# Performance work log

Measured on AMD Instinct MI355X. Metric: run time of the kernel, lower is better.

Reference implementation:

```python
import jax, jax.numpy as jnp
import numpy as np

B, L, E, H = 4, 2048, 512, 8
HD = E // H
EPS = 1e-6


def setup_inputs() -> dict:
    key = jax.random.key(0)
    ks = jax.random.split(key, 9)
    s = 0.02
    return {
        "query": jax.random.normal(ks[0], (B, L, E), dtype=jnp.float32),
        "Wq": jax.random.normal(ks[1], (E, E), dtype=jnp.float32) * s,
        "bq": jnp.zeros((E,), dtype=jnp.float32),
        "Wk": jax.random.normal(ks[2], (E, E), dtype=jnp.float32) * s,
        "bk": jnp.zeros((E,), dtype=jnp.float32),
        "Wv": jax.random.normal(ks[3], (E, E), dtype=jnp.float32) * s,
        "bv": jnp.zeros((E,), dtype=jnp.float32),
        "Wo": jax.random.normal(ks[4], (E, E), dtype=jnp.float32) * s,
        "bo": jnp.zeros((E,), dtype=jnp.float32),
    }


def reference(query, Wq, bq, Wk, bk, Wv, bv, Wo, bo):
    b, tgt_len, embed_dim = query.shape
    n_head = H
    head_dim = embed_dim // n_head
    # Faithful to the source: a raw view (reshape), NOT a transpose.
    x = query.reshape(tgt_len, b, embed_dim)  # (L, B, E)
    q = x @ Wq.T + bq
    k = x @ Wk.T + bk
    v = x @ Wv.T + bv
    # softmax over head_dim, per head
    q = jax.nn.softmax(q.reshape(tgt_len, b, n_head, head_dim), axis=-1)
    k = jax.nn.softmax(k.reshape(tgt_len, b, n_head, head_dim), axis=-1)
    # (L, B*H, hd) -> (B*H, L, hd)
    q_ = q.reshape(tgt_len, b * n_head, head_dim).swapaxes(0, 1)
    k_ = k.reshape(tgt_len, b * n_head, head_dim).swapaxes(0, 1)
    comp_q_ = 1.0 - q_
    comp_k_ = 1.0 - k_
    v_ = v.reshape(tgt_len, b * n_head, head_dim).swapaxes(0, 1)
    # non-causal XNor attention: scores from q.k^T + (1-q).(1-k)^T
    weights = jnp.einsum('nld,nsd->nls', q_, k_) + jnp.einsum('nld,nsd->nls', comp_q_, comp_k_)
    denom = jnp.clip(jnp.sum(weights, axis=-1, keepdims=True), EPS, None)
    attn_weights = weights / denom
    attn_output = jnp.einsum('nls,nsd->nld', attn_weights, v_)  # (B*H, L, hd)
    attn_output = attn_output.swapaxes(0, 1).reshape(tgt_len, b, embed_dim)
    out = attn_output @ Wo.T + bo
    return out.reshape(b, tgt_len, embed_dim)
```

## Files before the change

### kernel.cpp

```cpp
#include <hip/hip_runtime.h>

#define B_ 4
#define L_ 2048
#define E_ 512
#define H_ 8
#define NROW (B_*L_)
#define SZ (NROW*E_)
#define NH (B_*H_)

typedef unsigned short u16;
typedef unsigned int u32;
typedef __attribute__((ext_vector_type(8))) __bf16 bf16x8;
typedef __attribute__((ext_vector_type(8))) u16 u16x8;
typedef __attribute__((ext_vector_type(4))) float f32x4;

__device__ __forceinline__ u16 f2bf(float f) {
  union { float f; u32 u; } v; v.f = f;
  u32 r = v.u + 0x7FFFu + ((v.u >> 16) & 1u);
  return (u16)(r >> 16);
}
__device__ __forceinline__ float bf2f(u16 s) {
  union { u32 u; float f; } v; v.u = ((u32)s) << 16;
  return v.f;
}
__device__ __forceinline__ void async16(const u16* g, u16* l) {
  __builtin_amdgcn_global_load_lds(
      (const __attribute__((address_space(1))) u32*)g,
      (__attribute__((address_space(3))) u32*)l, 16, 0, 0);
}

__global__ __launch_bounds__(256) void cvt_all(const float* __restrict__ X,
    const float* __restrict__ W0, const float* __restrict__ W1,
    const float* __restrict__ W2, const float* __restrict__ W3,
    u16* __restrict__ Y, u16* __restrict__ Y0, u16* __restrict__ Y1,
    u16* __restrict__ Y2, u16* __restrict__ Y3) {
  const int bid = blockIdx.x;
  const float* src;
  u16* dst;
  int off;
  if (bid < 2048) { src = X; dst = Y; off = bid * 2048; }
  else {
    const int t = bid - 2048, s = t >> 7, r = t & 127;
    src = (s == 0) ? W0 : (s == 1) ? W1 : (s == 2) ? W2 : W3;
    dst = (s == 0) ? Y0 : (s == 1) ? Y1 : (s == 2) ? Y2 : Y3;
    off = r * 2048;
  }
  const int i0 = off + threadIdx.x * 8;
  f32x4 a = *(const f32x4*)(src + i0);
  f32x4 b = *(const f32x4*)(src + i0 + 4);
  u16x8 o;
#pragma unroll
  for (int j = 0; j < 4; ++j) { o[j] = f2bf(a[j]); o[4 + j] = f2bf(b[j]); }
  *(u16x8*)(dst + i0) = o;
}

__global__ __launch_bounds__(256, 3) void qkv_gemm(const u16* __restrict__ X,
    const u16* __restrict__ Wq, const u16* __restrict__ Wk, const u16* __restrict__ Wv,
    const float* __restrict__ bq, const float* __restrict__ bk, const float* __restrict__ bv,
    u16* __restrict__ Qo, u16* __restrict__ Ko, u16* __restrict__ Vo) {
  __shared__ __align__(16) union {
    struct { u16 a[2][128 * 32]; u16 b[2][128 * 32]; } st;
    u16 ep[4][16 * 72];
  } sh;
  const int z = blockIdx.z;
  const u16* W = (z == 0) ? Wq : (z == 1) ? Wk : Wv;
  const float* bias = (z == 0) ? bq : (z == 1) ? bk : bv;
  u16* C = (z == 0) ? Qo : (z == 1) ? Ko : Vo;
  const int tid = threadIdx.x;
  const int w = tid >> 6, lane = tid & 63;
  const int bm = blockIdx.x * 128, bn = blockIdx.y * 128;
  const int wm = (w >> 1) * 64, wn = (w & 1) * 64;
  const int fr = lane & 15, quad = lane >> 4;
  const int c0 = tid, c1 = tid + 256;
  const int ar0 = c0 >> 2, ak0 = (c0 & 3) * 8;
  const int ar1 = c1 >> 2, ak1 = (c1 & 3) * 8;
  f32x4 acc[4][4] = {};
  for (int k0 = 0; k0 < E_; k0 += 64) {
    __syncthreads();
#pragma unroll
    for (int p = 0; p < 2; ++p) {
      const int kp = k0 + p * 32;
      async16(X + (size_t)(bm + ar0) * E_ + kp + ak0, sh.st.a[p] + c0 * 8);
      async16(X + (size_t)(bm + ar1) * E_ + kp + ak1, sh.st.a[p] + c1 * 8);
      async16(W + (size_t)(bn + ar0) * E_ + kp + ak0, sh.st.b[p] + c0 * 8);
      async16(W + (size_t)(bn + ar1) * E_ + kp + ak1, sh.st.b[p] + c1 * 8);
    }
    __syncthreads();
#pragma unroll
    for (int p = 0; p < 2; ++p) {
      bf16x8 af[4], bf[4];
#pragma unroll
      for (int t = 0; t < 4; ++t) {
        af[t] = *(const bf16x8*)(sh.st.a[p] + (wm + t * 16 + fr) * 32 + quad * 8);
        bf[t] = *(const bf16x8*)(sh.st.b[p] + (wn + t * 16 + fr) * 32 + quad * 8);
      }
#pragma unroll
      for (int i = 0; i < 4; ++i)
#pragma unroll
        for (int j = 0; j < 4; ++j)
          acc[i][j] = __builtin_amdgcn_mfma_f32_16x16x32_bf16(af[i], bf[j], acc[i][j], 0, 0, 0);
    }
  }
  __syncthreads();
  u16* ep = sh.ep[w];
#pragma unroll
  for (int i = 0; i < 4; ++i) {
    if (z < 2) {
#pragma unroll
      for (int r = 0; r < 4; ++r) {
        float v[4];
#pragma unroll
        for (int nt = 0; nt < 4; ++nt)
          v[nt] = acc[i][nt][r] + bias[bn + wn + nt * 16 + fr];
        float e[4], ssum = 0.f;
#pragma unroll
        for (int nt = 0; nt < 4; ++nt) { e[nt] = __expf(v[nt]); ssum += e[nt]; }
#pragma unroll
        for (int off = 1; off < 16; off <<= 1) ssum += __shfl_xor(ssum, off, 64);
        const float inv = 1.f / ssum;
#pragma unroll
        for (int nt = 0; nt < 4; ++nt)
          ep[(quad * 4 + r) * 72 + nt * 16 + fr] = f2bf(e[nt] * inv);
      }
    } else {
#pragma unroll
      for (int r = 0; r < 4; ++r)
#pragma unroll
        for (int nt = 0; nt < 4; ++nt)
          ep[(quad * 4 + r) * 72 + nt * 16 + fr] =
              f2bf(acc[i][nt][r] + bias[bn + wn + nt * 16 + fr]);
    }
#pragma unroll
    for (int pass = 0; pass < 2; ++pass) {
      const int row = pass * 8 + (lane >> 3), ch = lane & 7;
      u16x8 val = *(const u16x8*)(ep + row * 72 + ch * 8);
      *(u16x8*)(C + (size_t)(bm + wm + i * 16 + row) * E_ + bn + wn + ch * 8) = val;
    }
  }
}

__global__ __launch_bounds__(256) void gemm_out(const u16* __restrict__ X,
    const u16* __restrict__ W, const float* __restrict__ bias, float* __restrict__ C) {
  __shared__ __align__(16) union {
    struct { u16 a[2][128 * 32]; u16 b[2][64 * 32]; } st;
    float ep[4][16 * 68];
  } sh;
  const int tid = threadIdx.x;
  const int w = tid >> 6, lane = tid & 63;
  const int bm = blockIdx.x * 128, bn = blockIdx.y * 64;
  const int fr = lane & 15, quad = lane >> 4;
  const int c0 = tid, c1 = tid + 256;
  const int ar0 = c0 >> 2, ak0 = (c0 & 3) * 8;
  const int ar1 = c1 >> 2, ak1 = (c1 & 3) * 8;
  f32x4 acc[2][4] = {};
  for (int k0 = 0; k0 < E_; k0 += 64) {
    __syncthreads();
#pragma unroll
    for (int p = 0; p < 2; ++p) {
      const int kp = k0 + p * 32;
      async16(X + (size_t)(bm + ar0) * E_ + kp + ak0, sh.st.a[p] + c0 * 8);
      async16(X + (size_t)(bm + ar1) * E_ + kp + ak1, sh.st.a[p] + c1 * 8);
      async16(W + (size_t)(bn + ar0) * E_ + kp + ak0, sh.st.b[p] + c0 * 8);
    }
    __syncthreads();
#pragma unroll
    for (int p = 0; p < 2; ++p) {
      bf16x8 af[2], bf[4];
#pragma unroll
      for (int mt = 0; mt < 2; ++mt)
        af[mt] = *(const bf16x8*)(sh.st.a[p] + (w * 32 + mt * 16 + fr) * 32 + quad * 8);
#pragma unroll
      for (int nt = 0; nt < 4; ++nt)
        bf[nt] = *(const bf16x8*)(sh.st.b[p] + (nt * 16 + fr) * 32 + quad * 8);
#pragma unroll
      for (int mt = 0; mt < 2; ++mt)
#pragma unroll
        for (int nt = 0; nt < 4; ++nt)
          acc[mt][nt] = __builtin_amdgcn_mfma_f32_16x16x32_bf16(af[mt], bf[nt],
                                                                acc[mt][nt], 0, 0, 0);
    }
  }
  __syncthreads();
  float* ep = sh.ep[w];
#pragma unroll
  for (int mt = 0; mt < 2; ++mt) {
#pragma unroll
    for (int r = 0; r < 4; ++r)
#pragma unroll
      for (int nt = 0; nt < 4; ++nt)
        ep[(quad * 4 + r) * 68 + nt * 16 + fr] = acc[mt][nt][r] + bias[bn + nt * 16 + fr];
#pragma unroll
    for (int p = 0; p < 4; ++p) {
      const int id = p * 64 + lane;
      const int row = id >> 4, ch = id & 15;
      f32x4 val = *(const f32x4*)(ep + row * 68 + ch * 4);
      *(f32x4*)(C + (size_t)(bm + w * 32 + mt * 16 + row) * E_ + bn + ch * 4) = val;
    }
  }
}

__global__ __launch_bounds__(64) void kv_part(const u16* __restrict__ K,
    const u16* __restrict__ V, float* __restrict__ Part,
    float* __restrict__ KPart, float* __restrict__ VPart) {
  __shared__ __align__(16) u16 sT[2][2][64 * 40];
  const int n = blockIdx.x, b = n >> 3, h = n & 7;
  const int sy = blockIdx.y;
  const int lane = threadIdx.x;
  const int lr = lane >> 1, half = lane & 1;
  const int fr = lane & 15, quad = lane >> 4;
  const int e0 = half * 32;
  f32x4 acc[4][4] = {};
  f32x4 accK[4] = {};
  f32x4 accV[4] = {};
  union { u16x8 u; bf16x8 b; } one;
#pragma unroll
  for (int j = 0; j < 8; ++j) one.u[j] = 0x3F80;
  u16x8 rK[4], rV[4], nK[4], nV[4];
  {
    const u16* gK = K + (size_t)((sy * 128 + lr) * B_ + b) * E_ + h * 64 + e0;
    const u16* gV = V + (size_t)((sy * 128 + lr) * B_ + b) * E_ + h * 64 + e0;
#pragma unroll
    for (int q = 0; q < 4; ++q) {
      rK[q] = *(const u16x8*)(gK + q * 8);
      rV[q] = *(const u16x8*)(gV + q * 8);
    }
  }
#pragma unroll
  for (int c = 0; c < 4; ++c) {
    const int buf = c & 1;
    u16* dK = &sT[buf][0][0];
    u16* dV = &sT[buf][1][0];
#pragma unroll
    for (int q = 0; q < 4; ++q)
#pragma unroll
      for (int j = 0; j < 8; ++j) {
        const int e = e0 + q * 8 + j;
        dK[e * 40 + lr] = rK[q][j];
        dV[e * 40 + lr] = rV[q][j];
      }
    if (c < 3) {
      const u16* gK = K + (size_t)((sy * 128 + (c + 1) * 32 + lr) * B_ + b) * E_ + h * 64 + e0;
      const u16* gV = V + (size_t)((sy * 128 + (c + 1) * 32 + lr) * B_ + b) * E_ + h * 64 + e0;
#pragma unroll
      for (int q = 0; q < 4; ++q) {
        nK[q] = *(const u16x8*)(gK + q * 8);
        nV[q] = *(const u16x8*)(gV + q * 8);
      }
    }
    bf16x8 af[4], bf[4];
#pragma unroll
    for (int t = 0; t < 4; ++t) {
      af[t] = *(const bf16x8*)(dV + (t * 16 + fr) * 40 + quad * 8);
      bf[t] = *(const bf16x8*)(dK + (t * 16 + fr) * 40 + quad * 8);
    }
#pragma unroll
    for (int i = 0; i < 4; ++i)
#pragma unroll
      for (int j = 0; j < 4; ++j)
        acc[i][j] = __builtin_amdgcn_mfma_f32_16x16x32_bf16(af[i], bf[j], acc[i][j], 0, 0, 0);
#pragma unroll
    for (int j = 0; j < 4; ++j)
      accK[j] = __builtin_amdgcn_mfma_f32_16x16x32_bf16(one.b, bf[j], accK[j], 0, 0, 0);
#pragma unroll
    for (int i = 0; i < 4; ++i)
      accV[i] = __builtin_amdgcn_mfma_f32_16x16x32_bf16(af[i], one.b, accV[i], 0, 0, 0);
#pragma unroll
    for (int q = 0; q < 4; ++q) { rK[q] = nK[q]; rV[q] = nV[q]; }
  }
  float* Pp = Part + (size_t)(n * 16 + sy) * 4096;
#pragma unroll
  for (int i = 0; i < 4; ++i)
#pragma unroll
    for (int j = 0; j < 4; ++j)
#pragma unroll
      for (int r = 0; r < 4; ++r)
        Pp[(i * 16 + quad * 4 + r) * 64 + j * 16 + fr] = acc[i][j][r];
  if (quad == 0) {
#pragma unroll
    for (int j = 0; j < 4; ++j)
      KPart[(n * 16 + sy) * 64 + j * 16 + fr] = accK[j][0];
  }
  if (fr == 0) {
#pragma unroll
    for (int i = 0; i < 4; ++i)
#pragma unroll
      for (int r = 0; r < 4; ++r)
        VPart[(n * 16 + sy) * 64 + i * 16 + quad * 4 + r] = accV[i][r];
  }
}

__global__ __launch_bounds__(256) void kv_merge(const float* __restrict__ Part,
    const float* __restrict__ KPart, const float* __restrict__ VPart,
    u16* __restrict__ Mtbf, float* __restrict__ Ks, float* __restrict__ Vs) {
  const int bid = blockIdx.x, tid = threadIdx.x;
  if (bid < 512) {
    const int oi = bid * 256 + tid;
    const int n = oi >> 12, j = oi & 4095;
    const float* p = Part + (size_t)n * 16 * 4096 + j;
    float s = 0.f;
#pragma unroll
    for (int sl = 0; sl < 16; ++sl) s += p[sl * 4096];
    Mtbf[oi] = f2bf(s);
  } else {
    const int i = (bid - 512) * 256 + tid;
    const int which = i >> 11, rem = i & 2047;
    const int n = rem >> 6, d = rem & 63;
    const float* p = (which ? VPart : KPart) + (n * 16) * 64 + d;
    float s = 0.f;
#pragma unroll
    for (int sl = 0; sl < 16; ++sl) s += p[sl * 64];
    if (which) Vs[n * 64 + d] = s; else Ks[n * 64 + d] = s;
  }
}

__global__ __launch_bounds__(256) void apply_mfma(const u16* __restrict__ Qbf,
    const u16* __restrict__ Mtbf, const float* __restrict__ Ksum,
    const float* __restrict__ Vsum, u16* __restrict__ Abf) {
  __shared__ __align__(16) u16 sQ[128 * 64];
  __shared__ __align__(16) u16 sM[64 * 64];
  __shared__ float sKs[64], sVs[64], sDen[128];
  const int n = blockIdx.x, b = n >> 3, h = n & 7;
  const int l0 = blockIdx.y * 128;
  const int tid = threadIdx.x, w = tid >> 6, lane = tid & 63;
  const int fr = lane & 15, quad = lane >> 4;
#pragma unroll
  for (int j = 0; j < 4; ++j) {
    const int rloc = w * 32 + j * 8;
    const int row = rloc + (lane >> 3);
    const int k = (lane & 7) * 8;
    async16(Qbf + (size_t)((l0 + row) * B_ + b) * E_ + h * 64 + k, sQ + rloc * 64);
  }
#pragma unroll
  for (int j = 0; j < 2; ++j) {
    const int c = j * 256 + tid;
    async16(Mtbf + (size_t)n * 4096 + c * 8, sM + c * 8);
  }
  if (tid < 64) sKs[tid] = Ksum[n * 64 + tid];
  else if (tid < 128) sVs[tid - 64] = Vsum[n * 64 + tid - 64];
  __syncthreads();
  union { u16x8 u; bf16x8 bv; } aU[2][2];
  bf16x8 bF[4][2];
#pragma unroll
  for (int mt = 0; mt < 2; ++mt)
#pragma unroll
    for (int ks = 0; ks < 2; ++ks)
      aU[mt][ks].u = *(const u16x8*)(sQ + (w * 32 + mt * 16 + fr) * 64 + ks * 32 + quad * 8);
#pragma unroll
  for (int nt = 0; nt < 4; ++nt)
#pragma unroll
    for (int ks = 0; ks < 2; ++ks)
      bF[nt][ks] = *(const bf16x8*)(sM + (nt * 16 + fr) * 64 + ks * 32 + quad * 8);
  float pden[2] = {0.f, 0.f};
#pragma unroll
  for (int mt = 0; mt < 2; ++mt)
#pragma unroll
    for (int ks = 0; ks < 2; ++ks)
#pragma unroll
      for (int j = 0; j < 8; ++j)
        pden[mt] = fmaf(bf2f(aU[mt][ks].u[j]), sKs[ks * 32 + quad * 8 + j], pden[mt]);
#pragma unroll
  for (int mt = 0; mt < 2; ++mt) {
    pden[mt] += __shfl_xor(pden[mt], 16, 64);
    pden[mt] += __shfl_xor(pden[mt], 32, 64);
    if (quad == 0)
      sDen[w * 32 + mt * 16 + fr] = fmaxf(2.f * pden[mt] + 62.f * (float)L_, 1e-6f);
  }
  __syncthreads();
  f32x4 acc[2][4];
#pragma unroll
  for (int mt = 0; mt < 2; ++mt)
#pragma unroll
    for (int nt = 0; nt < 4; ++nt) {
      const float iv = 31.f * sVs[nt * 16 + fr];
      acc[mt][nt] = (f32x4){iv, iv, iv, iv};
#pragma unroll
      for (int ks = 0; ks < 2; ++ks)
        acc[mt][nt] = __builtin_amdgcn_mfma_f32_16x16x32_bf16(aU[mt][ks].bv, bF[nt][ks],
                                                              acc[mt][nt], 0, 0, 0);
    }
#pragma unroll
  for (int mt = 0; mt < 2; ++mt)
#pragma unroll
    for (int r = 0; r < 4; ++r) {
      const int rloc = w * 32 + mt * 16 + quad * 4 + r;
      const float invd = 2.f / sDen[rloc];
      const size_t orow = (size_t)((l0 + rloc) * B_ + b) * E_ + h * 64;
#pragma unroll
      for (int nt = 0; nt < 4; ++nt)
        Abf[orow + nt * 16 + fr] = f2bf(acc[mt][nt][r] * invd);
    }
}

extern "C" void kernel_launch(void* const* d_in, const int* in_sizes, int n_in,
                              void* d_out, int out_size, void* d_ws, size_t ws_size,
                              hipStream_t stream) {
  const float* query = (const float*)d_in[0];
  const float* Wq = (const float*)d_in[1];
  const float* bq = (const float*)d_in[2];
  const float* Wk = (const float*)d_in[3];
  const float* bk = (const float*)d_in[4];
  const float* Wv = (const float*)d_in[5];
  const float* bv = (const float*)d_in[6];
  const float* Wo = (const float*)d_in[7];
  const float* bo = (const float*)d_in[8];
  float* out = (float*)d_out;

  char* ws = (char*)d_ws;
  u16* Xbf  = (u16*)(ws);
  u16* Qbf  = (u16*)(ws + 8388608);
  u16* Kbf  = (u16*)(ws + 16777216);
  u16* Vbf  = (u16*)(ws + 25165824);
  u16* Abf  = (u16*)(ws + 33554432);
  u16* Wqb  = (u16*)(ws + 41943040);
  u16* Wkb  = (u16*)(ws + 42467328);
  u16* Wvb  = (u16*)(ws + 42991616);
  u16* Wob  = (u16*)(ws + 43515904);
  u16* Mtbf = (u16*)(ws + 44040192);
  float* Ks = (float*)(ws + 44564480);
  float* Vs = (float*)(ws + 44572672);
  float* KPart = (float*)(ws + 44580864);
  float* VPart = (float*)(ws + 44711936);
  float* Part  = (float*)Xbf;

  cvt_all<<<2560, 256, 0, stream>>>(query, Wq, Wk, Wv, Wo,
                                    Xbf, Wqb, Wkb, Wvb, Wob);
  qkv_gemm<<<dim3(NROW / 128, E_ / 128, 3), 256, 0, stream>>>(
      Xbf, Wqb, Wkb, Wvb, bq, bk, bv, Qbf, Kbf, Vbf);
  kv_part<<<dim3(NH, 16), 64, 0, stream>>>(Kbf, Vbf, Part, KPart, VPart);
  kv_merge<<<528, 256, 0, stream>>>(Part, KPart, VPart, Mtbf, Ks, Vs);
  apply_mfma<<<dim3(NH, L_ / 128), 256, 0, stream>>>(Qbf, Mtbf, Ks, Vs, Abf);
  gemm_out<<<dim3(NROW / 128, E_ / 64), 256, 0, stream>>>(Abf, Wob, bo, out);
}
```

Measured before the change: 130.8 us.

## Fold output projection into per-head KV state to skip attention output buffer

The per-head K^T V state is transposed and multiplied by Wo in a new small kernel, giving a per-batch fused matrix G plus a bias-like V-sum term. The final GEMM then multiplies Q directly by G and computes the per-row denominator with an extra MFMA against the bf16 K sums, which removes the apply kernel and the round trip through the attention output buffer. The fused matrix is rounded to bf16, which may change accuracy, and the gemm_G kernel runs only 32 blocks.

```diff
diff --git a/kernel.cpp b/kernel.cpp
--- a/kernel.cpp
+++ b/kernel.cpp
@@ -139,66 +139,6 @@
   }
 }
 
-__global__ __launch_bounds__(256) void gemm_out(const u16* __restrict__ X,
-    const u16* __restrict__ W, const float* __restrict__ bias, float* __restrict__ C) {
-  __shared__ __align__(16) union {
-    struct { u16 a[2][128 * 32]; u16 b[2][64 * 32]; } st;
-    float ep[4][16 * 68];
-  } sh;
-  const int tid = threadIdx.x;
-  const int w = tid >> 6, lane = tid & 63;
-  const int bm = blockIdx.x * 128, bn = blockIdx.y * 64;
-  const int fr = lane & 15, quad = lane >> 4;
-  const int c0 = tid, c1 = tid + 256;
-  const int ar0 = c0 >> 2, ak0 = (c0 & 3) * 8;
-  const int ar1 = c1 >> 2, ak1 = (c1 & 3) * 8;
-  f32x4 acc[2][4] = {};
-  for (int k0 = 0; k0 < E_; k0 += 64) {
-    __syncthreads();
-#pragma unroll
-    for (int p = 0; p < 2; ++p) {
-      const int kp = k0 + p * 32;
-      async16(X + (size_t)(bm + ar0) * E_ + kp + ak0, sh.st.a[p] + c0 * 8);
-      async16(X + (size_t)(bm + ar1) * E_ + kp + ak1, sh.st.a[p] + c1 * 8);
-      async16(W + (size_t)(bn + ar0) * E_ + kp + ak0, sh.st.b[p] + c0 * 8);
-    }
-    __syncthreads();
-#pragma unroll
-    for (int p = 0; p < 2; ++p) {
-      bf16x8 af[2], bf[4];
-#pragma unroll
-      for (int mt = 0; mt < 2; ++mt)
-        af[mt] = *(const bf16x8*)(sh.st.a[p] + (w * 32 + mt * 16 + fr) * 32 + quad * 8);
-#pragma unroll
-      for (int nt = 0; nt < 4; ++nt)
-        bf[nt] = *(const bf16x8*)(sh.st.b[p] + (nt * 16 + fr) * 32 + quad * 8);
-#pragma unroll
-      for (int mt = 0; mt < 2; ++mt)
-#pragma unroll
-        for (int nt = 0; nt < 4; ++nt)
-          acc[mt][nt] = __builtin_amdgcn_mfma_f32_16x16x32_bf16(af[mt], bf[nt],
-                                                                acc[mt][nt], 0, 0, 0);
-    }
-  }
-  __syncthreads();
-  float* ep = sh.ep[w];
-#pragma unroll
-  for (int mt = 0; mt < 2; ++mt) {
-#pragma unroll
-    for (int r = 0; r < 4; ++r)
-#pragma unroll
-      for (int nt = 0; nt < 4; ++nt)
-        ep[(quad * 4 + r) * 68 + nt * 16 + fr] = acc[mt][nt][r] + bias[bn + nt * 16 + fr];
-#pragma unroll
-    for (int p = 0; p < 4; ++p) {
-      const int id = p * 64 + lane;
-      const int row = id >> 4, ch = id & 15;
-      f32x4 val = *(const f32x4*)(ep + row * 68 + ch * 4);
-      *(f32x4*)(C + (size_t)(bm + w * 32 + mt * 16 + row) * E_ + bn + ch * 4) = val;
-    }
-  }
-}
-
 __global__ __launch_bounds__(64) void kv_part(const u16* __restrict__ K,
     const u16* __restrict__ V, float* __restrict__ Part,
     float* __restrict__ KPart, float* __restrict__ VPart) {
@@ -250,8 +190,8 @@
     bf16x8 af[4], bf[4];
 #pragma unroll
     for (int t = 0; t < 4; ++t) {
-      af[t] = *(const bf16x8*)(dV + (t * 16 + fr) * 40 + quad * 8);
-      bf[t] = *(const bf16x8*)(dK + (t * 16 + fr) * 40 + quad * 8);
+      af[t] = *(const bf16x8*)(dK + (t * 16 + fr) * 40 + quad * 8);
+      bf[t] = *(const bf16x8*)(dV + (t * 16 + fr) * 40 + quad * 8);
     }
 #pragma unroll
     for (int i = 0; i < 4; ++i)
@@ -259,11 +199,11 @@
       for (int j = 0; j < 4; ++j)
         acc[i][j] = __builtin_amdgcn_mfma_f32_16x16x32_bf16(af[i], bf[j], acc[i][j], 0, 0, 0);
 #pragma unroll
+    for (int i = 0; i < 4; ++i)
+      accK[i] = __builtin_amdgcn_mfma_f32_16x16x32_bf16(af[i], one.b, accK[i], 0, 0, 0);
+#pragma unroll
     for (int j = 0; j < 4; ++j)
-      accK[j] = __builtin_amdgcn_mfma_f32_16x16x32_bf16(one.b, bf[j], accK[j], 0, 0, 0);
-#pragma unroll
-    for (int i = 0; i < 4; ++i)
-      accV[i] = __builtin_amdgcn_mfma_f32_16x16x32_bf16(af[i], one.b, accV[i], 0, 0, 0);
+      accV[j] = __builtin_amdgcn_mfma_f32_16x16x32_bf16(one.b, bf[j], accV[j], 0, 0, 0);
 #pragma unroll
     for (int q = 0; q < 4; ++q) { rK[q] = nK[q]; rV[q] = nV[q]; }
   }
@@ -275,23 +215,24 @@
 #pragma unroll
       for (int r = 0; r < 4; ++r)
         Pp[(i * 16 + quad * 4 + r) * 64 + j * 16 + fr] = acc[i][j][r];
+  if (fr == 0) {
+#pragma unroll
+    for (int i = 0; i < 4; ++i)
+#pragma unroll
+      for (int r = 0; r < 4; ++r)
+        KPart[(n * 16 + sy) * 64 + i * 16 + quad * 4 + r] = accK[i][r];
+  }
   if (quad == 0) {
 #pragma unroll
     for (int j = 0; j < 4; ++j)
-      KPart[(n * 16 + sy) * 64 + j * 16 + fr] = accK[j][0];
-  }
-  if (fr == 0) {
-#pragma unroll
-    for (int i = 0; i < 4; ++i)
-#pragma unroll
-      for (int r = 0; r < 4; ++r)
-        VPart[(n * 16 + sy) * 64 + i * 16 + quad * 4 + r] = accV[i][r];
+      VPart[(n * 16 + sy) * 64 + j * 16 + fr] = accV[j][0];
   }
 }
 
 __global__ __launch_bounds__(256) void kv_merge(const float* __restrict__ Part,
     const float* __restrict__ KPart, const float* __restrict__ VPart,
-    u16* __restrict__ Mtbf, float* __restrict__ Ks, float* __restrict__ Vs) {
+    u16* __restrict__ Mtbf, float* __restrict__ Ks, float* __restrict__ Vs,
+    u16* __restrict__ Ksb) {
   const int bid = blockIdx.x, tid = threadIdx.x;
   if (bid < 512) {
     const int oi = bid * 256 + tid;
@@ -309,86 +250,146 @@
     float s = 0.f;
 #pragma unroll
     for (int sl = 0; sl < 16; ++sl) s += p[sl * 64];
-    if (which) Vs[n * 64 + d] = s; else Ks[n * 64 + d] = s;
-  }
-}
-
-__global__ __launch_bounds__(256) void apply_mfma(const u16* __restrict__ Qbf,
-    const u16* __restrict__ Mtbf, const float* __restrict__ Ksum,
-    const float* __restrict__ Vsum, u16* __restrict__ Abf) {
-  __shared__ __align__(16) u16 sQ[128 * 64];
-  __shared__ __align__(16) u16 sM[64 * 64];
-  __shared__ float sKs[64], sVs[64], sDen[128];
+    if (which) Vs[n * 64 + d] = s;
+    else { Ks[n * 64 + d] = s; Ksb[n * 64 + d] = f2bf(s); }
+  }
+}
+
+__global__ __launch_bounds__(256) void gemm_G(const u16* __restrict__ Mtbf,
+    const u16* __restrict__ Wo, const float* __restrict__ Vs,
+    u16* __restrict__ Gt, float* __restrict__ Upart) {
+  __shared__ __align__(16) u16 ep[4][16 * 72];
   const int n = blockIdx.x, b = n >> 3, h = n & 7;
-  const int l0 = blockIdx.y * 128;
   const int tid = threadIdx.x, w = tid >> 6, lane = tid & 63;
   const int fr = lane & 15, quad = lane >> 4;
-#pragma unroll
-  for (int j = 0; j < 4; ++j) {
-    const int rloc = w * 32 + j * 8;
-    const int row = rloc + (lane >> 3);
-    const int k = (lane & 7) * 8;
-    async16(Qbf + (size_t)((l0 + row) * B_ + b) * E_ + h * 64 + k, sQ + rloc * 64);
-  }
-#pragma unroll
-  for (int j = 0; j < 2; ++j) {
-    const int c = j * 256 + tid;
-    async16(Mtbf + (size_t)n * 4096 + c * 8, sM + c * 8);
-  }
-  if (tid < 64) sKs[tid] = Ksum[n * 64 + tid];
-  else if (tid < 128) sVs[tid - 64] = Vsum[n * 64 + tid - 64];
+  const u16* Mn = Mtbf + (size_t)n * 4096;
+  f32x4 acc[8][4] = {};
+#pragma unroll
+  for (int ks = 0; ks < 2; ++ks) {
+    bf16x8 bfr[4];
+#pragma unroll
+    for (int j = 0; j < 4; ++j)
+      bfr[j] = *(const bf16x8*)(Mn + (j * 16 + fr) * 64 + ks * 32 + quad * 8);
+#pragma unroll
+    for (int i = 0; i < 8; ++i) {
+      bf16x8 afr = *(const bf16x8*)(Wo + (size_t)(w * 128 + i * 16 + fr) * E_ +
+                                    h * 64 + ks * 32 + quad * 8);
+#pragma unroll
+      for (int j = 0; j < 4; ++j)
+        acc[i][j] = __builtin_amdgcn_mfma_f32_16x16x32_bf16(afr, bfr[j], acc[i][j], 0, 0, 0);
+    }
+  }
+#pragma unroll
+  for (int t = 0; t < 2; ++t) {
+    const int f = t * 256 + tid;
+    const u16* wr = Wo + (size_t)f * E_ + h * 64;
+    float s = 0.f;
+#pragma unroll
+    for (int c = 0; c < 8; ++c) {
+      u16x8 v = *(const u16x8*)(wr + c * 8);
+#pragma unroll
+      for (int j = 0; j < 8; ++j) s = fmaf(bf2f(v[j]), Vs[n * 64 + c * 8 + j], s);
+    }
+    Upart[(size_t)n * 512 + f] = 62.f * s;
+  }
+  u16* e0 = ep[w];
+#pragma unroll
+  for (int i = 0; i < 8; ++i) {
+#pragma unroll
+    for (int j = 0; j < 4; ++j)
+#pragma unroll
+      for (int r = 0; r < 4; ++r)
+        e0[(quad * 4 + r) * 72 + j * 16 + fr] = f2bf(2.f * acc[i][j][r]);
+#pragma unroll
+    for (int pass = 0; pass < 2; ++pass) {
+      const int row = pass * 8 + (lane >> 3), ch = lane & 7;
+      u16x8 val = *(const u16x8*)(e0 + row * 72 + ch * 8);
+      *(u16x8*)(Gt + (size_t)(b * 512 + w * 128 + i * 16 + row) * E_ + h * 64 + ch * 8) = val;
+    }
+  }
+}
+
+__global__ __launch_bounds__(256) void final_gemm(const u16* __restrict__ Q,
+    const u16* __restrict__ Gt, const u16* __restrict__ Ksb,
+    const float* __restrict__ Upart, const float* __restrict__ bo,
+    float* __restrict__ C) {
+  __shared__ __align__(16) union {
+    struct { u16 a[2][128 * 32]; u16 b[2][64 * 32]; } st;
+    float ep[4][16 * 68];
+  } sh;
+  __shared__ __align__(16) u16 sKsb[512];
+  __shared__ float sU[64], sBo[64];
+  const int tid = threadIdx.x;
+  const int w = tid >> 6, lane = tid & 63;
+  const int bz = blockIdx.z;
+  const int l0 = blockIdx.x * 128, bn = blockIdx.y * 64;
+  const int fr = lane & 15, quad = lane >> 4;
+  const int c0 = tid, c1 = tid + 256;
+  const int ar0 = c0 >> 2, ak0 = (c0 & 3) * 8;
+  const int ar1 = c1 >> 2, ak1 = (c1 & 3) * 8;
+  const u16* Gb = Gt + (size_t)(bz * 512 + bn) * E_;
+  if (tid < 64) {
+    float s = 0.f;
+#pragma unroll
+    for (int hh = 0; hh < 8; ++hh) s += Upart[(size_t)(bz * 8 + hh) * 512 + bn + tid];
+    sU[tid] = s;
+    sBo[tid] = bo[bn + tid];
+  } else if (tid < 128) {
+    *(u16x8*)(sKsb + (tid - 64) * 8) = *(const u16x8*)(Ksb + bz * 512 + (tid - 64) * 8);
+  }
+  f32x4 acc[2][4] = {};
+  f32x4 accD[2] = {};
+  for (int k0 = 0; k0 < E_; k0 += 64) {
+    __syncthreads();
+#pragma unroll
+    for (int p = 0; p < 2; ++p) {
+      const int kp = k0 + p * 32;
+      async16(Q + (size_t)((l0 + ar0) * B_ + bz) * E_ + kp + ak0, sh.st.a[p] + c0 * 8);
+      async16(Q + (size_t)((l0 + ar1) * B_ + bz) * E_ + kp + ak1, sh.st.a[p] + c1 * 8);
+      async16(Gb + (size_t)ar0 * E_ + kp + ak0, sh.st.b[p] + c0 * 8);
+    }
+    __syncthreads();
+#pragma unroll
+    for (int p = 0; p < 2; ++p) {
+      bf16x8 af[2], bf[4];
+#pragma unroll
+      for (int mt = 0; mt < 2; ++mt)
+        af[mt] = *(const bf16x8*)(sh.st.a[p] + (w * 32 + mt * 16 + fr) * 32 + quad * 8);
+#pragma unroll
+      for (int nt = 0; nt < 4; ++nt)
+        bf[nt] = *(const bf16x8*)(sh.st.b[p] + (nt * 16 + fr) * 32 + quad * 8);
+      const bf16x8 bfK = *(const bf16x8*)(sKsb + k0 + p * 32 + quad * 8);
+#pragma unroll
+      for (int mt = 0; mt < 2; ++mt) {
+#pragma unroll
+        for (int nt = 0; nt < 4; ++nt)
+          acc[mt][nt] = __builtin_amdgcn_mfma_f32_16x16x32_bf16(af[mt], bf[nt],
+                                                                acc[mt][nt], 0, 0, 0);
+        accD[mt] = __builtin_amdgcn_mfma_f32_16x16x32_bf16(af[mt], bfK, accD[mt], 0, 0, 0);
+      }
+    }
+  }
   __syncthreads();
-  union { u16x8 u; bf16x8 bv; } aU[2][2];
-  bf16x8 bF[4][2];
-#pragma unroll
-  for (int mt = 0; mt < 2; ++mt)
-#pragma unroll
-    for (int ks = 0; ks < 2; ++ks)
-      aU[mt][ks].u = *(const u16x8*)(sQ + (w * 32 + mt * 16 + fr) * 64 + ks * 32 + quad * 8);
-#pragma unroll
-  for (int nt = 0; nt < 4; ++nt)
-#pragma unroll
-    for (int ks = 0; ks < 2; ++ks)
-      bF[nt][ks] = *(const bf16x8*)(sM + (nt * 16 + fr) * 64 + ks * 32 + quad * 8);
-  float pden[2] = {0.f, 0.f};
-#pragma unroll
-  for (int mt = 0; mt < 2; ++mt)
-#pragma unroll
-    for (int ks = 0; ks < 2; ++ks)
-#pragma unroll
-      for (int j = 0; j < 8; ++j)
-        pden[mt] = fmaf(bf2f(aU[mt][ks].u[j]), sKs[ks * 32 + quad * 8 + j], pden[mt]);
+  float* ep = sh.ep[w];
 #pragma unroll
   for (int mt = 0; mt < 2; ++mt) {
-    pden[mt] += __shfl_xor(pden[mt], 16, 64);
-    pden[mt] += __shfl_xor(pden[mt], 32, 64);
-    if (quad == 0)
-      sDen[w * 32 + mt * 16 + fr] = fmaxf(2.f * pden[mt] + 62.f * (float)L_, 1e-6f);
-  }
-  __syncthreads();
-  f32x4 acc[2][4];
-#pragma unroll
-  for (int mt = 0; mt < 2; ++mt)
-#pragma unroll
-    for (int nt = 0; nt < 4; ++nt) {
-      const float iv = 31.f * sVs[nt * 16 + fr];
-      acc[mt][nt] = (f32x4){iv, iv, iv, iv};
-#pragma unroll
-      for (int ks = 0; ks < 2; ++ks)
-        acc[mt][nt] = __builtin_amdgcn_mfma_f32_16x16x32_bf16(aU[mt][ks].bv, bF[nt][ks],
-                                                              acc[mt][nt], 0, 0, 0);
-    }
-#pragma unroll
-  for (int mt = 0; mt < 2; ++mt)
 #pragma unroll
     for (int r = 0; r < 4; ++r) {
-      const int rloc = w * 32 + mt * 16 + quad * 4 + r;
-      const float invd = 2.f / sDen[rloc];
-      const size_t orow = (size_t)((l0 + rloc) * B_ + b) * E_ + h * 64;
+      const float den = fmaxf(2.f * accD[mt][r] + 62.f * (float)L_, 1e-6f);
+      const float invd = 1.f / den;
 #pragma unroll
       for (int nt = 0; nt < 4; ++nt)
-        Abf[orow + nt * 16 + fr] = f2bf(acc[mt][nt][r] * invd);
-    }
+        ep[(quad * 4 + r) * 68 + nt * 16 + fr] =
+            (acc[mt][nt][r] + sU[nt * 16 + fr]) * invd + sBo[nt * 16 + fr];
+    }
+#pragma unroll
+    for (int p = 0; p < 4; ++p) {
+      const int id = p * 64 + lane;
+      const int row = id >> 4, ch = id & 15;
+      f32x4 val = *(const f32x4*)(ep + row * 68 + ch * 4);
+      *(f32x4*)(C + (size_t)((l0 + w * 32 + mt * 16 + row) * B_ + bz) * E_ + bn + ch * 4) = val;
+    }
+  }
 }
 
 extern "C" void kernel_launch(void* const* d_in, const int* in_sizes, int n_in,
@@ -410,7 +411,6 @@
   u16* Qbf  = (u16*)(ws + 8388608);
   u16* Kbf  = (u16*)(ws + 16777216);
   u16* Vbf  = (u16*)(ws + 25165824);
-  u16* Abf  = (u16*)(ws + 33554432);
   u16* Wqb  = (u16*)(ws + 41943040);
   u16* Wkb  = (u16*)(ws + 42467328);
   u16* Wvb  = (u16*)(ws + 42991616);
@@ -420,6 +420,9 @@
   float* Vs = (float*)(ws + 44572672);
   float* KPart = (float*)(ws + 44580864);
   float* VPart = (float*)(ws + 44711936);
+  u16* Gtb   = (u16*)(ws + 44843008);
+  float* Upart = (float*)(ws + 46940160);
+  u16* Ksb   = (u16*)(ws + 47005696);
   float* Part  = (float*)Xbf;
 
   cvt_all<<<2560, 256, 0, stream>>>(query, Wq, Wk, Wv, Wo,
@@ -427,7 +430,8 @@
   qkv_gemm<<<dim3(NROW / 128, E_ / 128, 3), 256, 0, stream>>>(
       Xbf, Wqb, Wkb, Wvb, bq, bk, bv, Qbf, Kbf, Vbf);
   kv_part<<<dim3(NH, 16), 64, 0, stream>>>(Kbf, Vbf, Part, KPart, VPart);
-  kv_merge<<<528, 256, 0, stream>>>(Part, KPart, VPart, Mtbf, Ks, Vs);
-  apply_mfma<<<dim3(NH, L_ / 128), 256, 0, stream>>>(Qbf, Mtbf, Ks, Vs, Abf);
-  gemm_out<<<dim3(NROW / 128, E_ / 64), 256, 0, stream>>>(Abf, Wob, bo, out);
-}
+  kv_merge<<<528, 256, 0, stream>>>(Part, KPart, VPart, Mtbf, Ks, Vs, Ksb);
+  gemm_G<<<NH, 256, 0, stream>>>(Mtbf, Wob, Vs, Gtb, Upart);
+  final_gemm<<<dim3(L_ / 128, E_ / 64, B_), 256, 0, stream>>>(
+      Qbf, Gtb, Ksb, Upart, bo, out);
+}
```

Result: slower. 134.3 us (+2.7%).

## Reduce KV partials in-block and fold merge into apply kernel

Applied to the files above, without the earlier changes.

kv_part now runs four waves per block, each handling 128 rows, and combines their partial K^T V, K-sum and V-sum accumulators through shared memory. This cuts the number of global partial slices from 16 to 4. The separate kv_merge launch is removed, and apply_mfma sums the 4 slices and converts them to bf16 directly into shared memory. The aim is to save a kernel launch and most of the partial-buffer traffic, at the cost of redundant merging in every apply block and fewer kv_part blocks (128 instead of 512).

```diff
diff --git a/kernel.cpp b/kernel.cpp
--- a/kernel.cpp
+++ b/kernel.cpp
@@ -199,16 +199,20 @@
   }
 }
 
-__global__ __launch_bounds__(64) void kv_part(const u16* __restrict__ K,
+__global__ __launch_bounds__(256) void kv_part(const u16* __restrict__ K,
     const u16* __restrict__ V, float* __restrict__ Part,
     float* __restrict__ KPart, float* __restrict__ VPart) {
-  __shared__ __align__(16) u16 sT[2][2][64 * 40];
+  __shared__ __align__(16) union {
+    u16 stg[4][2][2][64 * 40];
+    float red[3][64][100];
+  } sh;
   const int n = blockIdx.x, b = n >> 3, h = n & 7;
   const int sy = blockIdx.y;
-  const int lane = threadIdx.x;
+  const int tid = threadIdx.x, w = tid >> 6, lane = tid & 63;
   const int lr = lane >> 1, half = lane & 1;
   const int fr = lane & 15, quad = lane >> 4;
   const int e0 = half * 32;
+  const int row0 = sy * 512 + w * 128;
   f32x4 acc[4][4] = {};
   f32x4 accK[4] = {};
   f32x4 accV[4] = {};
@@ -217,8 +221,8 @@
   for (int j = 0; j < 8; ++j) one.u[j] = 0x3F80;
   u16x8 rK[4], rV[4], nK[4], nV[4];
   {
-    const u16* gK = K + (size_t)((sy * 128 + lr) * B_ + b) * E_ + h * 64 + e0;
-    const u16* gV = V + (size_t)((sy * 128 + lr) * B_ + b) * E_ + h * 64 + e0;
+    const u16* gK = K + (size_t)((row0 + lr) * B_ + b) * E_ + h * 64 + e0;
+    const u16* gV = V + (size_t)((row0 + lr) * B_ + b) * E_ + h * 64 + e0;
 #pragma unroll
     for (int q = 0; q < 4; ++q) {
       rK[q] = *(const u16x8*)(gK + q * 8);
@@ -228,8 +232,8 @@
 #pragma unroll
   for (int c = 0; c < 4; ++c) {
     const int buf = c & 1;
-    u16* dK = &sT[buf][0][0];
-    u16* dV = &sT[buf][1][0];
+    u16* dK = &sh.stg[w][buf][0][0];
+    u16* dV = &sh.stg[w][buf][1][0];
 #pragma unroll
     for (int q = 0; q < 4; ++q)
 #pragma unroll
@@ -239,8 +243,8 @@
         dV[e * 40 + lr] = rV[q][j];
       }
     if (c < 3) {
-      const u16* gK = K + (size_t)((sy * 128 + (c + 1) * 32 + lr) * B_ + b) * E_ + h * 64 + e0;
-      const u16* gV = V + (size_t)((sy * 128 + (c + 1) * 32 + lr) * B_ + b) * E_ + h * 64 + e0;
+      const u16* gK = K + (size_t)((row0 + (c + 1) * 32 + lr) * B_ + b) * E_ + h * 64 + e0;
+      const u16* gV = V + (size_t)((row0 + (c + 1) * 32 + lr) * B_ + b) * E_ + h * 64 + e0;
 #pragma unroll
       for (int q = 0; q < 4; ++q) {
         nK[q] = *(const u16x8*)(gK + q * 8);
@@ -267,55 +271,54 @@
 #pragma unroll
     for (int q = 0; q < 4; ++q) { rK[q] = nK[q]; rV[q] = nV[q]; }
   }
-  float* Pp = Part + (size_t)(n * 16 + sy) * 4096;
-#pragma unroll
-  for (int i = 0; i < 4; ++i)
-#pragma unroll
-    for (int j = 0; j < 4; ++j)
-#pragma unroll
-      for (int r = 0; r < 4; ++r)
-        Pp[(i * 16 + quad * 4 + r) * 64 + j * 16 + fr] = acc[i][j][r];
-  if (quad == 0) {
-#pragma unroll
-    for (int j = 0; j < 4; ++j)
-      KPart[(n * 16 + sy) * 64 + j * 16 + fr] = accK[j][0];
-  }
-  if (fr == 0) {
+  __syncthreads();
+  if (w > 0) {
+    float* rp = &sh.red[w - 1][lane][0];
+#pragma unroll
+    for (int t = 0; t < 16; ++t) *(f32x4*)(rp + t * 4) = acc[t >> 2][t & 3];
+#pragma unroll
+    for (int t = 0; t < 4; ++t) *(f32x4*)(rp + 64 + t * 4) = accK[t];
+#pragma unroll
+    for (int t = 0; t < 4; ++t) *(f32x4*)(rp + 80 + t * 4) = accV[t];
+  }
+  __syncthreads();
+  if (w == 0) {
+#pragma unroll
+    for (int p = 0; p < 3; ++p) {
+      const float* rp = &sh.red[p][lane][0];
+#pragma unroll
+      for (int t = 0; t < 16; ++t) acc[t >> 2][t & 3] += *(const f32x4*)(rp + t * 4);
+#pragma unroll
+      for (int t = 0; t < 4; ++t) accK[t] += *(const f32x4*)(rp + 64 + t * 4);
+#pragma unroll
+      for (int t = 0; t < 4; ++t) accV[t] += *(const f32x4*)(rp + 80 + t * 4);
+    }
+    float* Pp = Part + (size_t)(n * 4 + sy) * 4096;
 #pragma unroll
     for (int i = 0; i < 4; ++i)
 #pragma unroll
-      for (int r = 0; r < 4; ++r)
-        VPart[(n * 16 + sy) * 64 + i * 16 + quad * 4 + r] = accV[i][r];
-  }
-}
-
-__global__ __launch_bounds__(256) void kv_merge(const float* __restrict__ Part,
-    const float* __restrict__ KPart, const float* __restrict__ VPart,
-    u16* __restrict__ Mtbf, float* __restrict__ Ks, float* __restrict__ Vs) {
-  const int bid = blockIdx.x, tid = threadIdx.x;
-  if (bid < 512) {
-    const int oi = bid * 256 + tid;
-    const int n = oi >> 12, j = oi & 4095;
-    const float* p = Part + (size_t)n * 16 * 4096 + j;
-    float s = 0.f;
-#pragma unroll
-    for (int sl = 0; sl < 16; ++sl) s += p[sl * 4096];
-    Mtbf[oi] = f2bf(s);
-  } else {
-    const int i = (bid - 512) * 256 + tid;
-    const int which = i >> 11, rem = i & 2047;
-    const int n = rem >> 6, d = rem & 63;
-    const float* p = (which ? VPart : KPart) + (n * 16) * 64 + d;
-    float s = 0.f;
-#pragma unroll
-    for (int sl = 0; sl < 16; ++sl) s += p[sl * 64];
-    if (which) Vs[n * 64 + d] = s; else Ks[n * 64 + d] = s;
+      for (int j = 0; j < 4; ++j)
+#pragma unroll
+        for (int r = 0; r < 4; ++r)
+          Pp[(i * 16 + quad * 4 + r) * 64 + j * 16 + fr] = acc[i][j][r];
+    if (quad == 0) {
+#pragma unroll
+      for (int j = 0; j < 4; ++j)
+        KPart[(n * 4 + sy) * 64 + j * 16 + fr] = accK[j][0];
+    }
+    if (fr == 0) {
+#pragma unroll
+      for (int i = 0; i < 4; ++i)
+#pragma unroll
+        for (int r = 0; r < 4; ++r)
+          VPart[(n * 4 + sy) * 64 + i * 16 + quad * 4 + r] = accV[i][r];
+    }
   }
 }
 
 __global__ __launch_bounds__(256) void apply_mfma(const u16* __restrict__ Qbf,
-    const u16* __restrict__ Mtbf, const float* __restrict__ Ksum,
-    const float* __restrict__ Vsum, u16* __restrict__ Abf) {
+    const float* __restrict__ Part, const float* __restrict__ KPart,
+    const float* __restrict__ VPart, u16* __restrict__ Abf) {
   __shared__ __align__(16) u16 sQ[128 * 64];
   __shared__ __align__(16) u16 sM[64 * 64];
   __shared__ float sKs[64], sVs[64], sDen[128];
@@ -330,13 +333,38 @@
     const int k = (lane & 7) * 8;
     async16(Qbf + (size_t)((l0 + row) * B_ + b) * E_ + h * 64 + k, sQ + rloc * 64);
   }
-#pragma unroll
-  for (int j = 0; j < 2; ++j) {
-    const int c = j * 256 + tid;
-    async16(Mtbf + (size_t)n * 4096 + c * 8, sM + c * 8);
-  }
-  if (tid < 64) sKs[tid] = Ksum[n * 64 + tid];
-  else if (tid < 128) sVs[tid - 64] = Vsum[n * 64 + tid - 64];
+  {
+    const int e = tid >> 2, d0 = (tid & 3) * 16;
+    const float* Pp = Part + (size_t)n * 4 * 4096 + e * 64 + d0;
+    f32x4 s0 = {}, s1 = {}, s2 = {}, s3 = {};
+#pragma unroll
+    for (int s = 0; s < 4; ++s) {
+      const float* q = Pp + s * 4096;
+      s0 += *(const f32x4*)(q);
+      s1 += *(const f32x4*)(q + 4);
+      s2 += *(const f32x4*)(q + 8);
+      s3 += *(const f32x4*)(q + 12);
+    }
+    u16x8 o0, o1;
+#pragma unroll
+    for (int j = 0; j < 4; ++j) {
+      o0[j] = f2bf(s0[j]); o0[4 + j] = f2bf(s1[j]);
+      o1[j] = f2bf(s2[j]); o1[4 + j] = f2bf(s3[j]);
+    }
+    *(u16x8*)(sM + e * 64 + d0) = o0;
+    *(u16x8*)(sM + e * 64 + d0 + 8) = o1;
+  }
+  if (tid < 64) {
+    float s = 0.f;
+#pragma unroll
+    for (int sl = 0; sl < 4; ++sl) s += KPart[(n * 4 + sl) * 64 + tid];
+    sKs[tid] = s;
+  } else if (tid < 128) {
+    float s = 0.f;
+#pragma unroll
+    for (int sl = 0; sl < 4; ++sl) s += VPart[(n * 4 + sl) * 64 + tid - 64];
+    sVs[tid - 64] = s;
+  }
   __syncthreads();
   union { u16x8 u; bf16x8 bv; } aU[2][2];
   bf16x8 bF[4][2];
@@ -415,9 +443,6 @@
   u16* Wkb  = (u16*)(ws + 42467328);
   u16* Wvb  = (u16*)(ws + 42991616);
   u16* Wob  = (u16*)(ws + 43515904);
-  u16* Mtbf = (u16*)(ws + 44040192);
-  float* Ks = (float*)(ws + 44564480);
-  float* Vs = (float*)(ws + 44572672);
   float* KPart = (float*)(ws + 44580864);
   float* VPart = (float*)(ws + 44711936);
   float* Part  = (float*)Xbf;
@@ -426,8 +451,7 @@
                                     Xbf, Wqb, Wkb, Wvb, Wob);
   qkv_gemm<<<dim3(NROW / 128, E_ / 128, 3), 256, 0, stream>>>(
       Xbf, Wqb, Wkb, Wvb, bq, bk, bv, Qbf, Kbf, Vbf);
-  kv_part<<<dim3(NH, 16), 64, 0, stream>>>(Kbf, Vbf, Part, KPart, VPart);
-  kv_merge<<<528, 256, 0, stream>>>(Part, KPart, VPart, Mtbf, Ks, Vs);
-  apply_mfma<<<dim3(NH, L_ / 128), 256, 0, stream>>>(Qbf, Mtbf, Ks, Vs, Abf);
+  kv_part<<<dim3(NH, 4), 256, 0, stream>>>(Kbf, Vbf, Part, KPart, VPart);
+  apply_mfma<<<dim3(NH, L_ / 128), 256, 0, stream>>>(Qbf, Part, KPart, VPart, Abf);
   gemm_out<<<dim3(NROW / 128, E_ / 64), 256, 0, stream>>>(Abf, Wob, bo, out);
 }
```

After: 129.3 us (median of 2 runs). No clear change (-1.1%).
